# Optimization experiments

Measured on AMD Instinct MI355X. Metric: run time of the kernel, lower is better.

The kernel has to match this reference:

```python
import jax, jax.numpy as jnp
import numpy as np

N_NODES = 50000
N_EDGES = 800000
N_GRAPHS = 64
IN_DIM = 128
HID4 = 256  # hidden_dim * 4
OUT_DIM = 256
EPS = 1e-5


def setup_inputs() -> dict:
    key = jax.random.key(0)
    ks = jax.random.split(key, 11)
    x = jax.random.normal(ks[0], (N_NODES, IN_DIM), jnp.float32)
    w = jax.random.uniform(ks[1], (N_EDGES,), jnp.float32)
    src = jax.random.randint(ks[2], (N_EDGES,), 0, N_NODES, dtype=jnp.int32)
    dst = jax.random.randint(ks[3], (N_EDGES,), 0, N_NODES, dtype=jnp.int32)
    graph_ids = jnp.sort(jax.random.randint(ks[4], (N_NODES,), 0, N_GRAPHS, dtype=jnp.int32))
    W1 = jax.random.normal(ks[5], (IN_DIM, HID4), jnp.float32) * 0.05
    Wfc = jax.random.normal(ks[6], (IN_DIM, HID4), jnp.float32) * 0.05
    gamma = jnp.ones((HID4,), jnp.float32)
    beta = jnp.zeros((HID4,), jnp.float32)
    W2 = jax.random.normal(ks[7], (2 * HID4, HID4), jnp.float32) * 0.05
    W3 = jax.random.normal(ks[8], (HID4, OUT_DIM), jnp.float32) * 0.05
    return {"x": x, "w": w, "W1": W1, "Wfc": Wfc, "gamma": gamma, "beta": beta,
            "W2": W2, "W3": W3, "src": src, "dst": dst, "graph_ids": graph_ids}


def _agg(h, src, dst, w, n):
    # edge-weighted SpMM: sum_{e: dst(e)=v} w_e * h[src(e)]
    return jax.ops.segment_sum(h[src] * w[:, None], dst, num_segments=n)


def _graph_conv(h, W, src, dst, w, out_norm, in_norm, n):
    # DGL GraphConv, norm='both', no bias, with edge_weight.
    h = h * out_norm  # D_out^{-1/2} on source side
    din, dout = W.shape
    if din > dout:  # DGL applies W first when it shrinks the width
        h = _agg(h @ W, src, dst, w, n)
    else:
        h = _agg(h, src, dst, w, n) @ W
    return h * in_norm  # D_in^{-1/2} on destination side


def _layer_norm(h, gamma, beta):
    mu = jnp.mean(h, axis=-1, keepdims=True)
    var = jnp.var(h, axis=-1, keepdims=True)
    return (h - mu) * jax.lax.rsqrt(var + EPS) * gamma + beta


def reference(x, w, W1, Wfc, gamma, beta, W2, W3, src, dst, graph_ids):
    n = x.shape[0]
    ones_e = jnp.ones(src.shape[0], jnp.float32)
    out_deg = jnp.maximum(jax.ops.segment_sum(ones_e, src, num_segments=n), 1.0)
    in_deg = jnp.maximum(jax.ops.segment_sum(ones_e, dst, num_segments=n), 1.0)
    out_norm = (out_deg ** -0.5)[:, None]
    in_norm = (in_deg ** -0.5)[:, None]

    x1 = jax.nn.relu(_graph_conv(x, W1, src, dst, w, out_norm, in_norm, n))
    f1 = jax.nn.relu(_layer_norm(x @ Wfc, gamma, beta))
    x1f1 = jnp.concatenate((x1, f1), axis=1)  # [N, 512]
    x2 = jax.nn.relu(_graph_conv(x1f1, W2, src, dst, w, out_norm, in_norm, n))
    x3 = jax.nn.relu(_graph_conv(x2, W3, src, dst, w, out_norm, in_norm, n))
    # dgl.sum_nodes: per-graph segment-sum readout
    readout = jax.ops.segment_sum(x3, graph_ids, num_segments=N_GRAPHS)
    return readout
```

## Files before the change

### kernel.cpp

```cpp
#include <hip/hip_runtime.h>

#define NN 50000
#define NE 800000
#define NG 64
#define EPSF 1e-5f

typedef __bf16 bf16x8 __attribute__((ext_vector_type(8)));
typedef float f32x4 __attribute__((ext_vector_type(4)));

#define AS1 __attribute__((address_space(1)))
#define AS3 __attribute__((address_space(3)))

__device__ __forceinline__ void gl_lds16(const unsigned short* g, unsigned short* l) {
#if __has_builtin(__builtin_amdgcn_global_load_lds)
  __builtin_amdgcn_global_load_lds((const AS1 void*)g, (AS3 void*)l, 16, 0, 0);
#else
  *(uint4*)l = *(const uint4*)g;
#endif
}

__device__ __forceinline__ unsigned short f2bf(float f) {
  unsigned u = __builtin_bit_cast(unsigned, f);
  u += 0x7fff + ((u >> 16) & 1);
  return (unsigned short)(u >> 16);
}
__device__ __forceinline__ float bf_lo(unsigned u) {
  return __builtin_bit_cast(float, u << 16);
}
__device__ __forceinline__ float bf_hi(unsigned u) {
  return __builtin_bit_cast(float, u & 0xffff0000u);
}

#define NB_H 64
#define EC   12500
#define HWORDS 12500
#define XB   1563
#define XTOT 1600000
#define WTB  256
__global__ __launch_bounds__(1024) void prep_kernel(
    const int* __restrict__ src, const int* __restrict__ dst,
    unsigned char* __restrict__ hout, unsigned char* __restrict__ hin,
    int* __restrict__ rank,
    const float* __restrict__ x, unsigned short* __restrict__ xb,
    const float* __restrict__ W1, const float* __restrict__ Wfc,
    const float* __restrict__ W2, const float* __restrict__ W3,
    unsigned short* __restrict__ W1t, unsigned short* __restrict__ Wfct,
    unsigned short* __restrict__ W2t, unsigned short* __restrict__ W3t) {
  __shared__ unsigned hist[HWORDS];
  int b = blockIdx.x;
  int tid = threadIdx.x;
  if (b < NB_H) {
    int e0 = b * EC;
#pragma unroll
    for (int ph = 0; ph < 2; ph++) {
      const int* key = ph ? src : dst;
      unsigned char* gh = (ph ? hout : hin) + (size_t)b * NN;
      for (int i = tid; i < HWORDS; i += 1024) hist[i] = 0u;
      __syncthreads();
      for (int i = tid; i < EC; i += 1024) {
        int k = key[e0 + i];
        int sh = (k & 3) << 3;
        unsigned old = atomicAdd(&hist[k >> 2], 1u << sh);
        if (ph == 0) rank[e0 + i] = (int)((old >> sh) & 0xffu);
      }
      __syncthreads();
      unsigned* gw = (unsigned*)gh;
      for (int i = tid; i < HWORDS; i += 1024) gw[i] = hist[i];
      __syncthreads();
    }
  } else if (b < NB_H + XB) {
    int i = (b - NB_H) * 1024 + tid;
    if (i < XTOT) {
      float4 v = ((const float4*)x)[i];
      uint2 pk;
      pk.x = (unsigned)f2bf(v.x) | ((unsigned)f2bf(v.y) << 16);
      pk.y = (unsigned)f2bf(v.z) | ((unsigned)f2bf(v.w) << 16);
      ((uint2*)xb)[i] = pk;
    }
  } else {
    int i = (b - NB_H - XB) * 1024 + tid;
    const float* W; unsigned short* Wt; int K, local;
    if (i < 32768)       { W = W1;  Wt = W1t;  K = 128; local = i; }
    else if (i < 65536)  { W = Wfc; Wt = Wfct; K = 128; local = i - 32768; }
    else if (i < 196608) { W = W2;  Wt = W2t;  K = 512; local = i - 65536; }
    else                 { W = W3;  Wt = W3t;  K = 256; local = i - 196608; }
    int n = local / K, k = local - n * K;
    Wt[local] = f2bf(W[(size_t)k * 256 + n]);
  }
}

__global__ void norms_scan1(const unsigned char* __restrict__ hout,
                            unsigned char* __restrict__ hin,
                            int* __restrict__ din,
                            float* __restrict__ onorm, float* __restrict__ inorm,
                            int* __restrict__ bsum, int n) {
  int i = blockIdx.x * 256 + threadIdx.x;
  int d = 0;
  if (i < n) {
    int a = 0;
    for (int b = 0; b < NB_H; b++) a += hout[(size_t)b * NN + i];
    int run = 0;
    for (int b = 0; b < NB_H; b++) {
      int t = hin[(size_t)b * NN + i];
      hin[(size_t)b * NN + i] = (unsigned char)run;
      run += t;
    }
    d = run;
    din[i] = run;
    onorm[i] = rsqrtf((float)(a > 1 ? a : 1));
    inorm[i] = rsqrtf((float)(d > 1 ? d : 1));
  }
  int v = d;
#pragma unroll
  for (int off = 32; off > 0; off >>= 1) v += __shfl_down(v, off);
  __shared__ int ws[4];
  int wave = threadIdx.x >> 6, lane = threadIdx.x & 63;
  if (lane == 0) ws[wave] = v;
  __syncthreads();
  if (threadIdx.x == 0) bsum[blockIdx.x] = ws[0] + ws[1] + ws[2] + ws[3];
}

__global__ void scan3_kernel(const int* __restrict__ din, const int* __restrict__ bsum,
                             int* __restrict__ rp, int n, int nb) {
  int t = threadIdx.x;
  int lane = t & 63, wave = t >> 6;
  int bj = (t < nb) ? bsum[t] : 0;
  int pre = (t < (int)blockIdx.x) ? bj : 0;
  int p = pre, q = bj;
#pragma unroll
  for (int off = 32; off > 0; off >>= 1) {
    p += __shfl_down(p, off);
    q += __shfl_down(q, off);
  }
  __shared__ int red[8];
  __shared__ int baseS, totS;
  if (lane == 0) { red[wave] = p; red[4 + wave] = q; }
  __syncthreads();
  if (t == 0) {
    baseS = red[0] + red[1] + red[2] + red[3];
    totS  = red[4] + red[5] + red[6] + red[7];
  }
  __syncthreads();
  int i = blockIdx.x * 256 + t;
  int v = (i < n) ? din[i] : 0;
  __shared__ int tmp[256];
  tmp[t] = v;
  __syncthreads();
  for (int off = 1; off < 256; off <<= 1) {
    int x = (t >= off) ? tmp[t - off] : 0;
    __syncthreads();
    tmp[t] += x;
    __syncthreads();
  }
  if (i < n) rp[i] = tmp[t] - v + baseS;
  if (blockIdx.x == gridDim.x - 1 && t == 0) rp[n] = totS;
}

__global__ void fill_kernel(const int* __restrict__ src, const int* __restrict__ dst,
                            const float* __restrict__ w, const float* __restrict__ onorm,
                            const float* __restrict__ inorm,
                            const int* __restrict__ rp, const int* __restrict__ rank,
                            const unsigned char* __restrict__ binBase,
                            uint2* __restrict__ edge, int E) {
  int e = blockIdx.x * 256 + threadIdx.x;
  if (e < E) {
    int d = dst[e], s = src[e];
    int b = e / EC;
    int pos = rp[d] + (int)binBase[(size_t)b * NN + d] + rank[e];
    float wv = w[e] * onorm[s] * inorm[d];
    edge[pos] = make_uint2((unsigned)s, __builtin_bit_cast(unsigned, wv));
  }
}

template <int RELU, int NU>
__global__ __launch_bounds__(64) void spmm_bf16(
    const unsigned short* __restrict__ feat, int ldf,
    const int* __restrict__ rp, const uint2* __restrict__ edge,
    unsigned short* __restrict__ out, int ldo) {
  int v = blockIdx.x;
  int t = threadIdx.x;
  int beg = rp[v], end = rp[v + 1];
  float acc[2 * NU];
#pragma unroll
  for (int i = 0; i < 2 * NU; i++) acc[i] = 0.f;
  const unsigned short* base = feat + t * (2 * NU);
  int e = beg;
  for (; e + 8 <= end; e += 8) {
    int s[8]; float ww[8];
#pragma unroll
    for (int k = 0; k < 8; k++) {
      uint2 q = edge[e + k];
      s[k] = (int)q.x;
      ww[k] = __builtin_bit_cast(float, q.y);
    }
    unsigned u[8][NU];
#pragma unroll
    for (int k = 0; k < 8; k++) {
      const unsigned* pr = (const unsigned*)&base[(size_t)s[k] * ldf];
      if (NU == 2) { uint2 q = *(const uint2*)pr; u[k][0] = q.x; u[k][NU - 1] = q.y; }
      else u[k][0] = pr[0];
    }
#pragma unroll
    for (int k = 0; k < 8; k++)
#pragma unroll
      for (int j = 0; j < NU; j++) {
        acc[2 * j]     += ww[k] * bf_lo(u[k][j]);
        acc[2 * j + 1] += ww[k] * bf_hi(u[k][j]);
      }
  }
  for (; e < end; e++) {
    uint2 qe = edge[e];
    float w0 = __builtin_bit_cast(float, qe.y);
    const unsigned* pr = (const unsigned*)&base[(size_t)qe.x * ldf];
    unsigned u[NU];
    if (NU == 2) { uint2 q = *(const uint2*)pr; u[0] = q.x; u[NU - 1] = q.y; }
    else u[0] = pr[0];
#pragma unroll
    for (int j = 0; j < NU; j++) {
      acc[2 * j]     += w0 * bf_lo(u[j]);
      acc[2 * j + 1] += w0 * bf_hi(u[j]);
    }
  }
  unsigned o[NU];
#pragma unroll
  for (int j = 0; j < NU; j++) {
    float a = acc[2 * j], b = acc[2 * j + 1];
    if (RELU) { a = fmaxf(a, 0.f); b = fmaxf(b, 0.f); }
    o[j] = (unsigned)f2bf(a) | ((unsigned)f2bf(b) << 16);
  }
  unsigned* po = (unsigned*)&out[(size_t)v * ldo + t * (2 * NU)];
  if (NU == 2) *(uint2*)po = make_uint2(o[0], o[NU - 1]);
  else po[0] = o[0];
}

__device__ __forceinline__ void gemm_core(
    const unsigned short* __restrict__ A, int lda,
    const unsigned short* __restrict__ Bt, int K, int M,
    int bm, int bn, int relu,
    unsigned short (*As)[8192], unsigned short (*Bs)[8192],
    f32x4 (&acc)[4][4]) {
  const int tid = threadIdx.x;
  const int lane = tid & 63;
  const int m0 = bm * 128;
  const int n0 = bn * 128;

#pragma unroll
  for (int i = 0; i < 4; i++)
#pragma unroll
    for (int j = 0; j < 4; j++) acc[i][j] = (f32x4){0.f, 0.f, 0.f, 0.f};

  const unsigned short* pa[4];
  const unsigned short* pb[4];
#pragma unroll
  for (int i = 0; i < 4; i++) {
    int ch = i * 256 + tid;
    int sub = ch >> 6, sl = ch & 63;
    int mi = sub >> 1, kk = sub & 1;
    int row = mi * 16 + (sl & 15);
    int kc = kk * 32 + (sl >> 4) * 8;
    int gm = m0 + row; if (gm >= M) gm = M - 1;
    pa[i] = A + (size_t)gm * lda + kc;
    int gn = n0 + row;
    pb[i] = Bt + (size_t)gn * K + kc;
  }

  const int NT = K >> 6;
#pragma unroll
  for (int i = 0; i < 4; i++) {
    int ch8 = (i * 256 + tid) * 8;
    gl_lds16(pa[i], &As[0][ch8]);
    gl_lds16(pb[i], &Bs[0][ch8]);
  }
  __syncthreads();

  const int wv = tid >> 6;
  const int wm = wv >> 1, wn = wv & 1;
  int cur = 0;
  for (int t = 0; t < NT; t++) {
    if (t + 1 < NT) {
      int nk = (t + 1) << 6;
#pragma unroll
      for (int i = 0; i < 4; i++) {
        int ch8 = (i * 256 + tid) * 8;
        gl_lds16(pa[i] + nk, &As[cur ^ 1][ch8]);
        gl_lds16(pb[i] + nk, &Bs[cur ^ 1][ch8]);
      }
    }
#pragma unroll
    for (int kk = 0; kk < 2; kk++) {
      bf16x8 af[4], bfr[4];
#pragma unroll
      for (int i = 0; i < 4; i++)
        af[i] = *(const bf16x8*)&As[cur][((wm * 4 + i) * 2 + kk) * 512 + lane * 8];
#pragma unroll
      for (int j = 0; j < 4; j++)
        bfr[j] = *(const bf16x8*)&Bs[cur][((wn * 4 + j) * 2 + kk) * 512 + lane * 8];
#pragma unroll
      for (int i = 0; i < 4; i++)
#pragma unroll
        for (int j = 0; j < 4; j++)
          acc[i][j] = __builtin_amdgcn_mfma_f32_16x16x32_bf16(af[i], bfr[j], acc[i][j], 0, 0, 0);
    }
    __syncthreads();
    cur ^= 1;
  }
  if (relu) {
#pragma unroll
    for (int i = 0; i < 4; i++)
#pragma unroll
      for (int j = 0; j < 4; j++)
#pragma unroll
        for (int r = 0; r < 4; r++) acc[i][j][r] = fmaxf(acc[i][j][r], 0.f);
  }
}

__device__ __forceinline__ void gemm_store(
    const f32x4 (&acc)[4][4], unsigned short* __restrict__ C, int ldc,
    int col_off, int M, int bm, int bn) {
  const int tid = threadIdx.x;
  const int lane = tid & 63;
  const int wv = tid >> 6;
  const int wm = wv >> 1, wn = wv & 1;
  const int q = lane >> 4, r16 = lane & 15;
  const int m0 = bm * 128, n0 = bn * 128;
#pragma unroll
  for (int i = 0; i < 4; i++) {
    int rbase = m0 + wm * 64 + i * 16 + q * 4;
#pragma unroll
    for (int r = 0; r < 4; r++) {
      int gm = rbase + r;
      if (gm >= M) continue;
#pragma unroll
      for (int j = 0; j < 4; j++) {
        int gn = col_off + n0 + wn * 64 + j * 16 + r16;
        C[(size_t)gm * ldc + gn] = f2bf(acc[i][j][r]);
      }
    }
  }
}

__device__ __forceinline__ void fcln_body(
    const unsigned short* __restrict__ A, const unsigned short* __restrict__ Bt,
    const float* __restrict__ gamma, const float* __restrict__ beta,
    unsigned short* __restrict__ C, int M, unsigned short* lds) {
  const int tid = threadIdx.x;
  const int lane = tid & 63;
  const int w = tid >> 6;
  const int q = lane >> 4, r16 = lane & 15;
  const int m0 = blockIdx.x * 64;
  unsigned short* As = lds;
  unsigned short* Bs = lds + 8192;

#pragma unroll
  for (int i = 0; i < 4; i++) {
    int ch = i * 256 + tid;
    int st = ch >> 6, sl = ch & 63;
    int mi = st >> 2, kk = st & 3;
    int gm = m0 + mi * 16 + (sl & 15); if (gm >= M) gm = M - 1;
    int k = kk * 32 + (sl >> 4) * 8;
    gl_lds16(A + (size_t)gm * 128 + k, &As[ch * 8]);
  }
#pragma unroll
  for (int i = 0; i < 16; i++) {
    int ch = i * 256 + tid;
    int st = ch >> 6, sl = ch & 63;
    int ns = st >> 2, kk = st & 3;
    int n = ns * 16 + (sl & 15);
    int k = kk * 32 + (sl >> 4) * 8;
    gl_lds16(Bt + (size_t)n * 128 + k, &Bs[ch * 8]);
  }
  __syncthreads();

  f32x4 acc[4][4];
#pragma unroll
  for (int i = 0; i < 4; i++)
#pragma unroll
    for (int j = 0; j < 4; j++) acc[i][j] = (f32x4){0.f, 0.f, 0.f, 0.f};

#pragma unroll
  for (int kk = 0; kk < 4; kk++) {
    bf16x8 af[4], bfr[4];
#pragma unroll
    for (int i = 0; i < 4; i++)
      af[i] = *(const bf16x8*)&As[(i * 4 + kk) * 512 + lane * 8];
#pragma unroll
    for (int j = 0; j < 4; j++)
      bfr[j] = *(const bf16x8*)&Bs[((w * 4 + j) * 4 + kk) * 512 + lane * 8];
#pragma unroll
    for (int i = 0; i < 4; i++)
#pragma unroll
      for (int j = 0; j < 4; j++)
        acc[i][j] = __builtin_amdgcn_mfma_f32_16x16x32_bf16(af[i], bfr[j], acc[i][j], 0, 0, 0);
  }
  __syncthreads();

  float* fws = (float*)lds;
  float* fwq = fws + 256;
  float* fmean = fwq + 256;
  float* frs = fmean + 64;

#pragma unroll
  for (int i = 0; i < 4; i++)
#pragma unroll
    for (int r = 0; r < 4; r++) {
      float s  = acc[i][0][r] + acc[i][1][r] + acc[i][2][r] + acc[i][3][r];
      float q2 = acc[i][0][r] * acc[i][0][r] + acc[i][1][r] * acc[i][1][r] +
                 acc[i][2][r] * acc[i][2][r] + acc[i][3][r] * acc[i][3][r];
#pragma unroll
      for (int off = 8; off > 0; off >>= 1) {
        s  += __shfl_down(s, off, 16);
        q2 += __shfl_down(q2, off, 16);
      }
      if (r16 == 0) {
        int row = i * 16 + q * 4 + r;
        fws[w * 64 + row] = s;
        fwq[w * 64 + row] = q2;
      }
    }
  __syncthreads();
  if (tid < 64) {
    float S = fws[tid] + fws[64 + tid] + fws[128 + tid] + fws[192 + tid];
    float Q = fwq[tid] + fwq[64 + tid] + fwq[128 + tid] + fwq[192 + tid];
    float mean = S * (1.f / 256.f);
    float var = Q * (1.f / 256.f) - mean * mean;
    fmean[tid] = mean;
    frs[tid] = rsqrtf(var + EPSF);
  }
  __syncthreads();

  float g4[4], b4[4];
#pragma unroll
  for (int j = 0; j < 4; j++) {
    int c = w * 64 + j * 16 + r16;
    g4[j] = gamma[c];
    b4[j] = beta[c];
  }
#pragma unroll
  for (int i = 0; i < 4; i++)
#pragma unroll
    for (int r = 0; r < 4; r++) {
      int row = i * 16 + q * 4 + r;
      int gm = m0 + row;
      if (gm >= M) continue;
      float mean = fmean[row], rs = frs[row];
#pragma unroll
      for (int j = 0; j < 4; j++) {
        int c = w * 64 + j * 16 + r16;
        float y = (acc[i][j][r] - mean) * rs * g4[j] + b4[j];
        C[(size_t)gm * 512 + 256 + c] = f2bf(fmaxf(y, 0.f));
      }
    }
}

__global__ __launch_bounds__(256) void g12f_kernel(
    const unsigned short* __restrict__ A0, const unsigned short* __restrict__ B0,
    const unsigned short* __restrict__ A1, const unsigned short* __restrict__ B1,
    const float* __restrict__ gamma, const float* __restrict__ beta,
    unsigned short* __restrict__ C, int M) {
  __shared__ unsigned short lds[40960];
  if (blockIdx.z == 0) {
    f32x4 acc[4][4];
    int bm = blockIdx.x >> 1, bn = blockIdx.x & 1;
    gemm_core(A0, 128, B0, 128, M, bm, bn, 1,
              (unsigned short (*)[8192])lds,
              (unsigned short (*)[8192])(lds + 16384), acc);
    gemm_store(acc, C, 512, 0, M, bm, bn);
  } else {
    fcln_body(A1, B1, gamma, beta, C, M, lds);
  }
}

__global__ __launch_bounds__(256) void gemm_kernel(
    const unsigned short* __restrict__ A, int lda,
    const unsigned short* __restrict__ Bt, int K,
    unsigned short* __restrict__ C, int ldc, int M, int relu) {
  __shared__ unsigned short As[2][8192];
  __shared__ unsigned short Bs[2][8192];
  f32x4 acc[4][4];
  gemm_core(A, lda, Bt, K, M, blockIdx.x, blockIdx.y, relu, As, Bs, acc);
  gemm_store(acc, C, ldc, 0, M, blockIdx.x, blockIdx.y);
}

__global__ __launch_bounds__(256) void gemm_ro_kernel(
    const unsigned short* __restrict__ A,
    const unsigned short* __restrict__ Bt,
    const int* __restrict__ gid, float* __restrict__ part, int M) {
  __shared__ unsigned short As[2][8192];
  __shared__ unsigned short Bs[2][8192];
  __shared__ float red[4][128];
  f32x4 acc[4][4];
  gemm_core(A, 256, Bt, 256, M, blockIdx.x, blockIdx.y, 1, As, Bs, acc);

  const int tid = threadIdx.x;
  const int lane = tid & 63;
  const int wv = tid >> 6;
  const int wm = wv >> 1, wn = wv & 1;
  const int q = lane >> 4, r16 = lane & 15;
  const int m0 = blockIdx.x * 128;

  int g0 = gid[m0];
  int slots[4][4];
#pragma unroll
  for (int i = 0; i < 4; i++)
#pragma unroll
    for (int r = 0; r < 4; r++) {
      int gm = m0 + wm * 64 + i * 16 + q * 4 + r;
      slots[i][r] = (gm < M) ? gid[gm] - g0 : -1;
    }

  for (int idx = tid; idx < 512; idx += 256) ((float*)red)[idx] = 0.f;
  __syncthreads();
#pragma unroll
  for (int i = 0; i < 4; i++)
#pragma unroll
    for (int r = 0; r < 4; r++) {
      int sl = slots[i][r];
      if ((unsigned)sl < 4u) {
#pragma unroll
        for (int j = 0; j < 4; j++) {
          float v = acc[i][j][r];
          if (v != 0.f) atomicAdd(&red[sl][wn * 64 + j * 16 + r16], v);
        }
      }
    }
  __syncthreads();
  float* pp = part + ((size_t)(blockIdx.x * 2 + blockIdx.y) * 4) * 128;
  for (int idx = tid; idx < 512; idx += 256) pp[idx] = ((float*)red)[idx];
}

__global__ void readout_reduce(const float* __restrict__ part,
                               const int* __restrict__ gid,
                               float* __restrict__ out, int n) {
  int g = blockIdx.x;
  int c = threadIdx.x;
  int lo = 0, hi = n;
  while (lo < hi) { int mid = (lo + hi) >> 1; if (gid[mid] < g) lo = mid + 1; else hi = mid; }
  int s = lo;
  lo = s; hi = n;
  while (lo < hi) { int mid = (lo + hi) >> 1; if (gid[mid] < g + 1) lo = mid + 1; else hi = mid; }
  int e = lo;
  float acc = 0.f;
  if (s < e) {
    int bn = c >> 7, cc = c & 127;
    int bm0 = s >> 7, bm1 = (e - 1) >> 7;
    for (int bm = bm0; bm <= bm1; bm++) {
      int sl = g - gid[bm * 128];
      if ((unsigned)sl < 4u)
        acc += part[(((size_t)bm * 2 + bn) * 4 + sl) * 128 + cc];
    }
  }
  out[g * 256 + c] = acc;
}


extern "C" void kernel_launch(void* const* d_in, const int* in_sizes, int n_in,
                              void* d_out, int out_size, void* d_ws, size_t ws_size,
                              hipStream_t stream) {
  const float* x     = (const float*)d_in[0];
  const float* w     = (const float*)d_in[1];
  const float* W1    = (const float*)d_in[2];
  const float* Wfc   = (const float*)d_in[3];
  const float* gamma = (const float*)d_in[4];
  const float* beta  = (const float*)d_in[5];
  const float* W2    = (const float*)d_in[6];
  const float* W3    = (const float*)d_in[7];
  const int*   src   = (const int*)d_in[8];
  const int*   dst   = (const int*)d_in[9];
  const int*   gid   = (const int*)d_in[10];
  float* out = (float*)d_out;

  const int N = NN, E = NE;

  char* p = (char*)d_ws;
  auto alloc = [&](size_t bytes) {
    char* r = p;
    p += (bytes + 255) & ~(size_t)255;
    return r;
  };
  unsigned char* hout = (unsigned char*)alloc((size_t)NB_H * N);
  unsigned char* hin  = (unsigned char*)alloc((size_t)NB_H * N);
  int*   din     = (int*)alloc((size_t)N * 4);
  float* onorm   = (float*)alloc((size_t)N * 4);
  float* inorm   = (float*)alloc((size_t)N * 4);
  int*   row_ptr = (int*)alloc((size_t)(N + 1) * 4);
  int*   bsum    = (int*)alloc(256 * 4);
  int*   rank    = (int*)alloc((size_t)E * 4);
  uint2* edge    = (uint2*)alloc((size_t)E * 8);
  float* part    = (float*)alloc((size_t)391 * 2 * 4 * 128 * 4);
  unsigned short* xb    = (unsigned short*)alloc((size_t)N * 128 * 2);
  unsigned short* aggX  = (unsigned short*)alloc((size_t)N * 128 * 2);
  unsigned short* x1f1  = (unsigned short*)alloc((size_t)N * 512 * 2);
  unsigned short* y2    = (unsigned short*)alloc((size_t)N * 256 * 2);
  unsigned short* x2    = (unsigned short*)alloc((size_t)N * 256 * 2);
  unsigned short* aggx2 = (unsigned short*)alloc((size_t)N * 256 * 2);
  unsigned short* W1t   = (unsigned short*)alloc((size_t)256 * 128 * 2);
  unsigned short* Wfct  = (unsigned short*)alloc((size_t)256 * 128 * 2);
  unsigned short* W2t   = (unsigned short*)alloc((size_t)256 * 512 * 2);
  unsigned short* W3t   = (unsigned short*)alloc((size_t)256 * 256 * 2);

  const int nbS = (N + 255) / 256;

  prep_kernel<<<NB_H + XB + WTB, 1024, 0, stream>>>(src, dst, hout, hin, rank,
                                                    x, xb, W1, Wfc, W2, W3,
                                                    W1t, Wfct, W2t, W3t);
  norms_scan1<<<nbS, 256, 0, stream>>>(hout, hin, din, onorm, inorm, bsum, N);
  scan3_kernel<<<nbS, 256, 0, stream>>>(din, bsum, row_ptr, N, nbS);
  fill_kernel<<<(E + 255) / 256, 256, 0, stream>>>(src, dst, w, onorm, inorm, row_ptr,
                                                   rank, hin, edge, E);

  dim3 ggrid((N + 127) / 128, 2);

  spmm_bf16<0, 1><<<N, 64, 0, stream>>>(xb, 128, row_ptr, edge, aggX, 128);
  g12f_kernel<<<dim3(782, 1, 2), 256, 0, stream>>>(aggX, W1t, xb, Wfct, gamma, beta, x1f1, N);
  gemm_kernel<<<ggrid, 256, 0, stream>>>(x1f1, 512, W2t, 512, y2, 256, N, 0);
  spmm_bf16<1, 2><<<N, 64, 0, stream>>>(y2, 256, row_ptr, edge, x2, 256);
  spmm_bf16<0, 2><<<N, 64, 0, stream>>>(x2, 256, row_ptr, edge, aggx2, 256);
  gemm_ro_kernel<<<ggrid, 256, 0, stream>>>(aggx2, W3t, gid, part, N);
  readout_reduce<<<NG, 256, 0, stream>>>(part, gid, out, N);
}
```

Measured before the change: 420.1 us.

## Fuse final SpMM with W3 GEMM and readout into one kernel

Replaces the separate third-layer aggregation kernel and the GEMM+readout kernel with one kernel. Each block aggregates 16 destination rows into LDS as bf16 MFMA A-fragments, multiplies by W3 with 16x16x32 MFMA, applies ReLU and reduces into per-graph partials. This removes the write and reread of the N×256 aggregated intermediate and one launch. In exchange, B tiles are read straight from global memory by every block (3125 blocks), the tile per block is small, and the partial buffer grows, so the readout reduce scans more entries.

```diff
diff --git a/kernel.cpp b/kernel.cpp
--- a/kernel.cpp
+++ b/kernel.cpp
@@ -481,51 +481,99 @@
   gemm_store(acc, C, ldc, 0, M, blockIdx.x, blockIdx.y);
 }
 
-__global__ __launch_bounds__(256) void gemm_ro_kernel(
-    const unsigned short* __restrict__ A,
+__global__ __launch_bounds__(256) void spmm_gemm_ro(
+    const unsigned short* __restrict__ x2,
+    const int* __restrict__ rp, const uint2* __restrict__ edge,
     const unsigned short* __restrict__ Bt,
-    const int* __restrict__ gid, float* __restrict__ part, int M) {
-  __shared__ unsigned short As[2][8192];
-  __shared__ unsigned short Bs[2][8192];
-  __shared__ float red[4][128];
-  f32x4 acc[4][4];
-  gemm_core(A, 256, Bt, 256, M, blockIdx.x, blockIdx.y, 1, As, Bs, acc);
-
+    const int* __restrict__ gid, float* __restrict__ part) {
+  __shared__ unsigned short As[8 * 512];
+  __shared__ float red[4][256];
   const int tid = threadIdx.x;
-  const int lane = tid & 63;
-  const int wv = tid >> 6;
-  const int wm = wv >> 1, wn = wv & 1;
-  const int q = lane >> 4, r16 = lane & 15;
-  const int m0 = blockIdx.x * 128;
-
-  int g0 = gid[m0];
-  int slots[4][4];
-#pragma unroll
-  for (int i = 0; i < 4; i++)
-#pragma unroll
-    for (int r = 0; r < 4; r++) {
-      int gm = m0 + wm * 64 + i * 16 + q * 4 + r;
-      slots[i][r] = (gm < M) ? gid[gm] - g0 : -1;
-    }
-
-  for (int idx = tid; idx < 512; idx += 256) ((float*)red)[idx] = 0.f;
-  __syncthreads();
-#pragma unroll
-  for (int i = 0; i < 4; i++)
-#pragma unroll
-    for (int r = 0; r < 4; r++) {
-      int sl = slots[i][r];
-      if ((unsigned)sl < 4u) {
-#pragma unroll
-        for (int j = 0; j < 4; j++) {
-          float v = acc[i][j][r];
-          if (v != 0.f) atomicAdd(&red[sl][wn * 64 + j * 16 + r16], v);
-        }
-      }
-    }
-  __syncthreads();
-  float* pp = part + ((size_t)(blockIdx.x * 2 + blockIdx.y) * 4) * 128;
-  for (int idx = tid; idx < 512; idx += 256) pp[idx] = ((float*)red)[idx];
+  const int l = tid & 63;
+  const int w = tid >> 6;
+  const int v0 = blockIdx.x * 16;
+
+  for (int i = tid; i < 1024; i += 256) ((float*)red)[i] = 0.f;
+
+  const unsigned short* base = x2 + l * 4;
+  const int kt_w = l >> 3;
+  const int lf_w = 16 * ((l & 7) >> 1);
+  const int off4 = 4 * (l & 1);
+  for (int i = 0; i < 4; i++) {
+    int r = w * 4 + i;
+    int v = v0 + r;
+    int beg = rp[v], end = rp[v + 1];
+    float a0 = 0.f, a1 = 0.f, a2 = 0.f, a3 = 0.f;
+    int e = beg;
+    for (; e + 8 <= end; e += 8) {
+      int s[8]; float ww[8];
+#pragma unroll
+      for (int k = 0; k < 8; k++) {
+        uint2 q = edge[e + k];
+        s[k] = (int)q.x;
+        ww[k] = __builtin_bit_cast(float, q.y);
+      }
+      unsigned u[8][2];
+#pragma unroll
+      for (int k = 0; k < 8; k++) {
+        uint2 q = *(const uint2*)&base[(size_t)s[k] * 256];
+        u[k][0] = q.x; u[k][1] = q.y;
+      }
+#pragma unroll
+      for (int k = 0; k < 8; k++) {
+        a0 += ww[k] * bf_lo(u[k][0]);
+        a1 += ww[k] * bf_hi(u[k][0]);
+        a2 += ww[k] * bf_lo(u[k][1]);
+        a3 += ww[k] * bf_hi(u[k][1]);
+      }
+    }
+    for (; e < end; e++) {
+      uint2 qe = edge[e];
+      float w0 = __builtin_bit_cast(float, qe.y);
+      uint2 q = *(const uint2*)&base[(size_t)qe.x * 256];
+      a0 += w0 * bf_lo(q.x);
+      a1 += w0 * bf_hi(q.x);
+      a2 += w0 * bf_lo(q.y);
+      a3 += w0 * bf_hi(q.y);
+    }
+    unsigned p0 = (unsigned)f2bf(a0) | ((unsigned)f2bf(a1) << 16);
+    unsigned p1 = (unsigned)f2bf(a2) | ((unsigned)f2bf(a3) << 16);
+    *(uint2*)&As[kt_w * 512 + (r + lf_w) * 8 + off4] = make_uint2(p0, p1);
+  }
+  __syncthreads();
+
+  bf16x8 af[8];
+#pragma unroll
+  for (int kt = 0; kt < 8; kt++)
+    af[kt] = *(const bf16x8*)&As[kt * 512 + l * 8];
+
+  const int r16 = l & 15, q = l >> 4;
+  int g0 = gid[v0];
+  int slot[4];
+#pragma unroll
+  for (int j = 0; j < 4; j++) slot[j] = gid[v0 + q * 4 + j] - g0;
+
+#pragma unroll
+  for (int nt = 0; nt < 4; nt++) {
+    int nrow = (w * 4 + nt) * 16 + r16;
+    const unsigned short* pb = Bt + (size_t)nrow * 256 + q * 8;
+    f32x4 acc = (f32x4){0.f, 0.f, 0.f, 0.f};
+#pragma unroll
+    for (int kt = 0; kt < 8; kt++) {
+      bf16x8 bf = *(const bf16x8*)&pb[kt * 32];
+      acc = __builtin_amdgcn_mfma_f32_16x16x32_bf16(af[kt], bf, acc, 0, 0, 0);
+    }
+#pragma unroll
+    for (int j = 0; j < 4; j++) {
+      float vv = fmaxf(acc[j], 0.f);
+      int sl = slot[j];
+      if (vv != 0.f && (unsigned)sl < 4u)
+        atomicAdd(&red[sl][(w * 4 + nt) * 16 + r16], vv);
+    }
+  }
+  __syncthreads();
+  float* pp = part + (size_t)blockIdx.x * 1024;
+  for (int i = tid; i < 1024; i += 256) pp[i] = ((float*)red)[i];
 }
 
 __global__ void readout_reduce(const float* __restrict__ part,
@@ -541,12 +589,11 @@
   int e = lo;
   float acc = 0.f;
   if (s < e) {
-    int bn = c >> 7, cc = c & 127;
-    int bm0 = s >> 7, bm1 = (e - 1) >> 7;
-    for (int bm = bm0; bm <= bm1; bm++) {
-      int sl = g - gid[bm * 128];
+    int b0 = s >> 4, b1 = (e - 1) >> 4;
+    for (int b = b0; b <= b1; b++) {
+      int sl = g - gid[b * 16];
       if ((unsigned)sl < 4u)
-        acc += part[(((size_t)bm * 2 + bn) * 4 + sl) * 128 + cc];
+        acc += part[(size_t)b * 1024 + sl * 256 + c];
     }
   }
   out[g * 256 + c] = acc;
@@ -586,13 +633,12 @@
   int*   bsum    = (int*)alloc(256 * 4);
   int*   rank    = (int*)alloc((size_t)E * 4);
   uint2* edge    = (uint2*)alloc((size_t)E * 8);
-  float* part    = (float*)alloc((size_t)391 * 2 * 4 * 128 * 4);
+  float* part    = (float*)alloc((size_t)3125 * 4 * 256 * 4);
   unsigned short* xb    = (unsigned short*)alloc((size_t)N * 128 * 2);
   unsigned short* aggX  = (unsigned short*)alloc((size_t)N * 128 * 2);
   unsigned short* x1f1  = (unsigned short*)alloc((size_t)N * 512 * 2);
   unsigned short* y2    = (unsigned short*)alloc((size_t)N * 256 * 2);
   unsigned short* x2    = (unsigned short*)alloc((size_t)N * 256 * 2);
-  unsigned short* aggx2 = (unsigned short*)alloc((size_t)N * 256 * 2);
   unsigned short* W1t   = (unsigned short*)alloc((size_t)256 * 128 * 2);
   unsigned short* Wfct  = (unsigned short*)alloc((size_t)256 * 128 * 2);
   unsigned short* W2t   = (unsigned short*)alloc((size_t)256 * 512 * 2);
@@ -614,7 +660,6 @@
   g12f_kernel<<<dim3(782, 1, 2), 256, 0, stream>>>(aggX, W1t, xb, Wfct, gamma, beta, x1f1, N);
   gemm_kernel<<<ggrid, 256, 0, stream>>>(x1f1, 512, W2t, 512, y2, 256, N, 0);
   spmm_bf16<1, 2><<<N, 64, 0, stream>>>(y2, 256, row_ptr, edge, x2, 256);
-  spmm_bf16<0, 2><<<N, 64, 0, stream>>>(x2, 256, row_ptr, edge, aggx2, 256);
-  gemm_ro_kernel<<<ggrid, 256, 0, stream>>>(aggx2, W3t, gid, part, N);
+  spmm_gemm_ro<<<3125, 256, 0, stream>>>(x2, row_ptr, edge, W3t, gid, part);
   readout_reduce<<<NG, 256, 0, stream>>>(part, gid, out, N);
 }
```

Measured after the change: 427.1 us. About the same (+1.6%).

## Replace tiled readout GEMM with register-resident per-wave MFMA and pre-reduced atomics

Applied to the files above, without the earlier changes.

The final GEMM+readout kernel no longer uses the shared LDS-tiled 128x128 gemm_core. Each wave now keeps a 16-row A slice in registers and streams all of W3t straight from global memory, using 16x16x32 bf16 MFMAs over 782 blocks of 64 rows. The ReLU'd results are summed across the four rows a lane holds when they share a graph, which cuts LDS atomics. The aim is to drop LDS staging and sync overhead and raise block count. In exchange every wave re-reads the whole weight matrix from global/L2, the partial buffer is larger, and the readout reduce is changed to match.

```diff
diff --git a/kernel.cpp b/kernel.cpp
--- a/kernel.cpp
+++ b/kernel.cpp
@@ -481,51 +481,66 @@
   gemm_store(acc, C, ldc, 0, M, blockIdx.x, blockIdx.y);
 }
 
-__global__ __launch_bounds__(256) void gemm_ro_kernel(
+__global__ __launch_bounds__(256) void gemm_ro2(
     const unsigned short* __restrict__ A,
     const unsigned short* __restrict__ Bt,
     const int* __restrict__ gid, float* __restrict__ part, int M) {
-  __shared__ unsigned short As[2][8192];
-  __shared__ unsigned short Bs[2][8192];
-  __shared__ float red[4][128];
-  f32x4 acc[4][4];
-  gemm_core(A, 256, Bt, 256, M, blockIdx.x, blockIdx.y, 1, As, Bs, acc);
-
+  __shared__ float red[4][256];
   const int tid = threadIdx.x;
-  const int lane = tid & 63;
-  const int wv = tid >> 6;
-  const int wm = wv >> 1, wn = wv & 1;
-  const int q = lane >> 4, r16 = lane & 15;
-  const int m0 = blockIdx.x * 128;
-
-  int g0 = gid[m0];
-  int slots[4][4];
-#pragma unroll
-  for (int i = 0; i < 4; i++)
-#pragma unroll
-    for (int r = 0; r < 4; r++) {
-      int gm = m0 + wm * 64 + i * 16 + q * 4 + r;
-      slots[i][r] = (gm < M) ? gid[gm] - g0 : -1;
-    }
-
-  for (int idx = tid; idx < 512; idx += 256) ((float*)red)[idx] = 0.f;
-  __syncthreads();
-#pragma unroll
-  for (int i = 0; i < 4; i++)
-#pragma unroll
-    for (int r = 0; r < 4; r++) {
-      int sl = slots[i][r];
-      if ((unsigned)sl < 4u) {
-#pragma unroll
-        for (int j = 0; j < 4; j++) {
-          float v = acc[i][j][r];
-          if (v != 0.f) atomicAdd(&red[sl][wn * 64 + j * 16 + r16], v);
-        }
-      }
-    }
-  __syncthreads();
-  float* pp = part + ((size_t)(blockIdx.x * 2 + blockIdx.y) * 4) * 128;
-  for (int idx = tid; idx < 512; idx += 256) pp[idx] = ((float*)red)[idx];
+  const int l = tid & 63;
+  const int w = tid >> 6;
+  const int v0 = blockIdx.x * 64;
+  const int vw = v0 + w * 16;
+
+  for (int i = tid; i < 1024; i += 256) ((float*)red)[i] = 0.f;
+  __syncthreads();
+
+  const int r16 = l & 15, q = l >> 4;
+  int arow = vw + r16; if (arow >= M) arow = M - 1;
+  const unsigned short* pa = A + (size_t)arow * 256 + q * 8;
+  bf16x8 af[8];
+#pragma unroll
+  for (int kt = 0; kt < 8; kt++)
+    af[kt] = *(const bf16x8*)&pa[kt * 32];
+
+  int g0 = gid[v0];
+  int slot[4];
+#pragma unroll
+  for (int j = 0; j < 4; j++) {
+    int gm = vw + q * 4 + j;
+    slot[j] = (gm < M) ? gid[gm] - g0 : -1;
+  }
+  bool uni = (slot[0] == slot[3]);
+
+  const unsigned short* pb0 = Bt + (size_t)r16 * 256 + q * 8;
+#pragma unroll 4
+  for (int nt = 0; nt < 16; nt++) {
+    const unsigned short* pb = pb0 + (size_t)(nt * 16) * 256;
+    f32x4 acc = (f32x4){0.f, 0.f, 0.f, 0.f};
+#pragma unroll
+    for (int kt = 0; kt < 8; kt++) {
+      bf16x8 bf = *(const bf16x8*)&pb[kt * 32];
+      acc = __builtin_amdgcn_mfma_f32_16x16x32_bf16(af[kt], bf, acc, 0, 0, 0);
+    }
+    int col = nt * 16 + r16;
+    if (uni) {
+      if ((unsigned)slot[0] < 4u) {
+        float s = fmaxf(acc[0], 0.f) + fmaxf(acc[1], 0.f) +
+                  fmaxf(acc[2], 0.f) + fmaxf(acc[3], 0.f);
+        atomicAdd(&red[slot[0]][col], s);
+      }
+    } else {
+#pragma unroll
+      for (int j = 0; j < 4; j++) {
+        float vv = fmaxf(acc[j], 0.f);
+        int sl = slot[j];
+        if ((unsigned)sl < 4u && vv != 0.f) atomicAdd(&red[sl][col], vv);
+      }
+    }
+  }
+  __syncthreads();
+  float* pp = part + (size_t)blockIdx.x * 1024;
+  for (int i = tid; i < 1024; i += 256) pp[i] = ((float*)red)[i];
 }
 
 __global__ void readout_reduce(const float* __restrict__ part,
@@ -541,12 +556,11 @@
   int e = lo;
   float acc = 0.f;
   if (s < e) {
-    int bn = c >> 7, cc = c & 127;
-    int bm0 = s >> 7, bm1 = (e - 1) >> 7;
-    for (int bm = bm0; bm <= bm1; bm++) {
-      int sl = g - gid[bm * 128];
+    int b0 = s >> 6, b1 = (e - 1) >> 6;
+    for (int b = b0; b <= b1; b++) {
+      int sl = g - gid[b * 64];
       if ((unsigned)sl < 4u)
-        acc += part[(((size_t)bm * 2 + bn) * 4 + sl) * 128 + cc];
+        acc += part[(size_t)b * 1024 + sl * 256 + c];
     }
   }
   out[g * 256 + c] = acc;
@@ -586,7 +600,7 @@
   int*   bsum    = (int*)alloc(256 * 4);
   int*   rank    = (int*)alloc((size_t)E * 4);
   uint2* edge    = (uint2*)alloc((size_t)E * 8);
-  float* part    = (float*)alloc((size_t)391 * 2 * 4 * 128 * 4);
+  float* part    = (float*)alloc((size_t)782 * 4 * 256 * 4);
   unsigned short* xb    = (unsigned short*)alloc((size_t)N * 128 * 2);
   unsigned short* aggX  = (unsigned short*)alloc((size_t)N * 128 * 2);
   unsigned short* x1f1  = (unsigned short*)alloc((size_t)N * 512 * 2);
@@ -615,6 +629,6 @@
   gemm_kernel<<<ggrid, 256, 0, stream>>>(x1f1, 512, W2t, 512, y2, 256, N, 0);
   spmm_bf16<1, 2><<<N, 64, 0, stream>>>(y2, 256, row_ptr, edge, x2, 256);
   spmm_bf16<0, 2><<<N, 64, 0, stream>>>(x2, 256, row_ptr, edge, aggx2, 256);
-  gemm_ro_kernel<<<ggrid, 256, 0, stream>>>(aggx2, W3t, gid, part, N);
+  gemm_ro2<<<782, 256, 0, stream>>>(aggx2, W3t, gid, part, N);
   readout_reduce<<<NG, 256, 0, stream>>>(part, gid, out, N);
 }
```

After: 415.1 us. About the same (-1.2%).
